# Kernel optimization log

Hardware: AMD Instinct MI355X
Metric: run time of the kernel (lower is better)

Reference implementation:

```python
import jax, jax.numpy as jnp
import numpy as np

N, E, D, H, ED = 10000, 160000, 512, 256, 16
EPS = 1e-5  # BatchNorm1d eps


def _cgconv(x, src, dst, edge_attr, Wf, bf, Ws, bs, gamma, beta, mean, var):
    # PyG CGConv: z = [x_i, x_j, e_ij]; m = sigmoid(lin_f(z)) * softplus(lin_s(z));
    # aggr='add' at target i; batch_norm (eval mode, running stats) then residual.
    z = jnp.concatenate([x[dst], x[src], edge_attr], axis=1)  # [E, 2D+ED]
    m = jax.nn.sigmoid(z @ Wf + bf) * jax.nn.softplus(z @ Ws + bs)  # [E, D]
    aggr = jax.ops.segment_sum(m, dst, num_segments=x.shape[0])  # [N, D]
    bn = (aggr - mean) * jax.lax.rsqrt(var + EPS) * gamma + beta
    return x + bn


def _gcnconv(x, src, dst, W, b):
    # PyG GCNConv with add_self_loops=True, normalize=True:
    n = x.shape[0]
    deg = jax.ops.segment_sum(jnp.ones((src.shape[0],), x.dtype), dst, num_segments=n) + 1.0
    dinv = jax.lax.rsqrt(deg)  # [N]
    h = x @ W  # [N, out]
    out = jax.ops.segment_sum((dinv[src] * dinv[dst])[:, None] * h[src], dst, num_segments=n)
    out = out + (dinv * dinv)[:, None] * h  # self-loop contribution
    return out + b


def _forward(x, edge_attr, goal_feat,
             cg1_Wf, cg1_bf, cg1_Ws, cg1_bs, cg1_gamma, cg1_beta, cg1_mean, cg1_var,
             cg2_Wf, cg2_bf, cg2_Ws, cg2_bs, cg2_gamma, cg2_beta, cg2_mean, cg2_var,
             gcn3_W, gcn3_b, gcn4_W, gcn4_b, d1_W, d1_b, d2_W, d2_b, src, dst):
    # dropout layers are identity in eval mode (self.training=False)
    x = jax.nn.relu(_cgconv(x, src, dst, edge_attr, cg1_Wf, cg1_bf, cg1_Ws, cg1_bs,
                            cg1_gamma, cg1_beta, cg1_mean, cg1_var))
    x = jax.nn.relu(_cgconv(x, src, dst, edge_attr, cg2_Wf, cg2_bf, cg2_Ws, cg2_bs,
                            cg2_gamma, cg2_beta, cg2_mean, cg2_var))
    x = jax.nn.relu(_gcnconv(x, src, dst, gcn3_W, gcn3_b))
    x = jax.nn.relu(_gcnconv(x, src, dst, gcn4_W, gcn4_b))
    g = jnp.broadcast_to(goal_feat, (x.shape[0], goal_feat.shape[1]))  # repeat(num_nodes, 1)
    h = jax.nn.relu(jnp.concatenate([x, g], axis=1) @ d1_W + d1_b)
    return h @ d2_W + d2_b  # [N, 1]


def setup_inputs() -> dict:
    ks = jax.random.split(jax.random.key(0), 12)
    w = lambda k, s: jax.random.normal(k, s, dtype=jnp.float32) * 0.02
    Z = 2 * D + ED
    return {
        "x": jax.random.normal(ks[0], (N, D), jnp.float32),
        "edge_attr": jax.random.normal(ks[1], (E, ED), jnp.float32),
        "goal_feat": jax.random.normal(ks[2], (1, D), jnp.float32),
        "cg1_Wf": w(ks[3], (Z, D)), "cg1_bf": jnp.zeros((D,), jnp.float32),
        "cg1_Ws": w(ks[4], (Z, D)), "cg1_bs": jnp.zeros((D,), jnp.float32),
        "cg1_gamma": jnp.ones((D,), jnp.float32), "cg1_beta": jnp.zeros((D,), jnp.float32),
        "cg1_mean": jnp.zeros((D,), jnp.float32), "cg1_var": jnp.ones((D,), jnp.float32),
        "cg2_Wf": w(ks[5], (Z, D)), "cg2_bf": jnp.zeros((D,), jnp.float32),
        "cg2_Ws": w(ks[6], (Z, D)), "cg2_bs": jnp.zeros((D,), jnp.float32),
        "cg2_gamma": jnp.ones((D,), jnp.float32), "cg2_beta": jnp.zeros((D,), jnp.float32),
        "cg2_mean": jnp.zeros((D,), jnp.float32), "cg2_var": jnp.ones((D,), jnp.float32),
        "gcn3_W": w(ks[7], (D, H)), "gcn3_b": jnp.zeros((H,), jnp.float32),
        "gcn4_W": w(ks[8], (H, H)), "gcn4_b": jnp.zeros((H,), jnp.float32),
        "d1_W": w(ks[9], (H + D, D)), "d1_b": jnp.zeros((D,), jnp.float32),
        "d2_W": w(ks[10], (D, 1)), "d2_b": jnp.zeros((1,), jnp.float32),
        "edge_index": jax.random.randint(ks[11], (2, E), 0, N, dtype=jnp.int32),
        "batch": jnp.zeros((N,), jnp.int32),
    }


def reference(x, edge_attr, goal_feat,
              cg1_Wf, cg1_bf, cg1_Ws, cg1_bs, cg1_gamma, cg1_beta, cg1_mean, cg1_var,
              cg2_Wf, cg2_bf, cg2_Ws, cg2_bs, cg2_gamma, cg2_beta, cg2_mean, cg2_var,
              gcn3_W, gcn3_b, gcn4_W, gcn4_b, d1_W, d1_b, d2_W, d2_b,
              edge_index, batch):
    src, dst = edge_index[0], edge_index[1]
    return _forward(x, edge_attr, goal_feat,
                    cg1_Wf, cg1_bf, cg1_Ws, cg1_bs, cg1_gamma, cg1_beta, cg1_mean, cg1_var,
                    cg2_Wf, cg2_bf, cg2_Ws, cg2_bs, cg2_gamma, cg2_beta, cg2_mean, cg2_var,
                    gcn3_W, gcn3_b, gcn4_W, gcn4_b, d1_W, d1_b, d2_W, d2_b, src, dst)
```

## Files before the change

kernel.cpp:

```cpp
#include <hip/hip_runtime.h>
#include <math.h>

#define N_NODES 10000
#define N_EDGES 160000
#define DIM 512
#define HDIM 256
#define EDIM 16
#define BN_EPS 1e-5f
#define L2E 1.4426950408889634f
#define LN2 0.6931471805599453f

typedef unsigned short ushort_t;
typedef unsigned int uint_t;
typedef __attribute__((ext_vector_type(8))) short bf16x8;
typedef __attribute__((ext_vector_type(4))) float f32x4;
typedef __attribute__((ext_vector_type(2))) _Float16 half2_t;

__device__ __forceinline__ ushort_t f2bf(float x) {
    uint_t u = __float_as_uint(x);
    uint_t r = (u + 0x7FFF + ((u >> 16) & 1)) >> 16;
    return (ushort_t)r;
}
__device__ __forceinline__ float bflo(uint_t u) {
    return __uint_as_float(u << 16);
}
__device__ __forceinline__ float bfhi(uint_t u) {
    return __uint_as_float(u & 0xffff0000u);
}
__device__ __forceinline__ void gld16(const void* g, void* l) {
    __builtin_amdgcn_global_load_lds(
        (const __attribute__((address_space(1))) unsigned int*)g,
        (__attribute__((address_space(3))) unsigned int*)l, 16, 0, 0);
}
__device__ __forceinline__ half2_t u2h(uint_t u) {
    return __builtin_bit_cast(half2_t, u);
}
__device__ __forceinline__ uint_t pk_f16(float a, float b) {
    return __builtin_bit_cast(uint_t, __builtin_amdgcn_cvt_pkrtz(a, b));
}
__device__ __forceinline__ ushort_t f2h(float x) {
    return (ushort_t)(pk_f16(x, 0.f) & 0xffffu);
}
__device__ __forceinline__ float fexp2(float x) {
#if __has_builtin(__builtin_amdgcn_exp2f)
    return __builtin_amdgcn_exp2f(x);
#else
    return __expf(x * LN2);
#endif
}
__device__ __forceinline__ float flog2(float x) {
#if __has_builtin(__builtin_amdgcn_logf)
    return __builtin_amdgcn_logf(x);
#else
    return __logf(x) * L2E;
#endif
}
__device__ __forceinline__ void swz(int lid, int gx, int gy, int& bx, int& by) {
    int per = gy * 8;
    int grp = lid / per;
    int rem = lid - grp * per;
    int gsz = min(8, gx - grp * 8);
    by = rem / gsz;
    bx = grp * 8 + (rem - by * gsz);
}

__global__ void k_hist(const int* __restrict__ dst, int* __restrict__ cnt) {
    int e = blockIdx.x * blockDim.x + threadIdx.x;
    if (e < N_EDGES) atomicAdd(&cnt[dst[e]], 1);
}

__global__ __launch_bounds__(1024) void k_scan(int* __restrict__ offs, float* __restrict__ dinv) {
    __shared__ int wsum[16];
    int t = threadIdx.x, lane = t & 63, wv = t >> 6;
    int base_i = t * 10;
    int v[10];
    int s = 0;
#pragma unroll
    for (int k = 0; k < 10; k++) {
        int idx = base_i + k;
        int x = (idx < N_NODES) ? offs[idx] : 0;
        v[k] = x;
        s += x;
        if (idx < N_NODES) dinv[idx] = rsqrtf((float)x + 1.0f);
    }
    int ps = s;
#pragma unroll
    for (int off = 1; off < 64; off <<= 1) {
        int u = __shfl_up(ps, off, 64);
        if (lane >= off) ps += u;
    }
    if (lane == 63) wsum[wv] = ps;
    __syncthreads();
    if (wv == 0) {
        int w = (lane < 16) ? wsum[lane] : 0;
#pragma unroll
        for (int off = 1; off < 16; off <<= 1) {
            int u = __shfl_up(w, off, 64);
            if (lane >= off) w += u;
        }
        if (lane < 16) wsum[lane] = w;
    }
    __syncthreads();
    int wbase = (wv == 0) ? 0 : wsum[wv - 1];
    int run = wbase + ps - s;
#pragma unroll
    for (int k = 0; k < 10; k++) {
        int idx = base_i + k;
        if (idx < N_NODES) offs[idx] = run;
        run += v[k];
    }
    if (t == 1023) offs[N_NODES] = wsum[15];
}

__global__ void k_scatter(const int* __restrict__ srcv, const int* __restrict__ dstv,
                          const float* __restrict__ ea,
                          const int* __restrict__ offs, const float* __restrict__ dinv,
                          int* __restrict__ cursor,
                          int* __restrict__ srcQ, int* __restrict__ srcH,
                          float* __restrict__ dinvArr,
                          uint_t* __restrict__ eaP) {
    int e = blockIdx.x * blockDim.x + threadIdx.x;
    if (e >= N_EDGES) return;
    int d = dstv[e];
    int p = offs[d] + atomicAdd(&cursor[d], 1);
    int s = srcv[e];
    srcQ[p] = s << 11;
    srcH[p] = s << 9;
    dinvArr[p] = dinv[s];
    const float* er = ea + (size_t)e * EDIM;
    uint_t pk[8];
#pragma unroll
    for (int k2 = 0; k2 < 8; k2++) pk[k2] = pk_f16(er[2 * k2], er[2 * k2 + 1]);
    uint_t* q = eaP + (size_t)p * 8;
    *(uint4*)q = *(uint4*)&pk[0];
    *(uint4*)(q + 4) = *(uint4*)&pk[4];
}

__global__ __launch_bounds__(256) void k_cvtW(
    const float* __restrict__ Wf0, const float* __restrict__ Ws0,
    const float* __restrict__ Wf1, const float* __restrict__ Ws1,
    const float* __restrict__ g3W, const float* __restrict__ g4W,
    const float* __restrict__ d1W,
    ushort_t* __restrict__ W2cg0, ushort_t* __restrict__ W2cg1,
    ushort_t* __restrict__ W2g3, ushort_t* __restrict__ W2g4,
    ushort_t* __restrict__ W2d1)
{
    __shared__ ushort_t tle[64][72];
    int b = blockIdx.x, t = threadIdx.x;
    const float* src; int ldw, kin0, cin0, ldk, cout0, kout0; ushort_t* out; float scale;
    if (b < 512) {
        int layer = b >> 8, tt = b & 255;
        int g = tt >> 6, rem = tt & 63;
        int ct = rem >> 3, kt = rem & 7;
        const float* Wf = layer ? Wf1 : Wf0;
        const float* Ws = layer ? Ws1 : Ws0;
        src = (g & 1) ? Ws : Wf;
        ldw = 512; kin0 = ((g & 2) ? 512 : 0) + kt * 64; cin0 = ct * 64;
        out = layer ? W2cg1 : W2cg0; ldk = 512;
        cout0 = g * 512 + ct * 64; kout0 = kt * 64;
        scale = L2E;
    } else if (b < 544) {
        int tt = b - 512; int ct = tt >> 3, kt = tt & 7;
        src = g3W; ldw = 256; kin0 = kt * 64; cin0 = ct * 64;
        out = W2g3; ldk = 512; cout0 = ct * 64; kout0 = kt * 64; scale = 1.f;
    } else if (b < 560) {
        int tt = b - 544; int ct = tt >> 2, kt = tt & 3;
        src = g4W; ldw = 256; kin0 = kt * 64; cin0 = ct * 64;
        out = W2g4; ldk = 256; cout0 = ct * 64; kout0 = kt * 64; scale = 1.f;
    } else {
        int tt = b - 560; int ct = tt >> 2, kt = tt & 3;
        src = d1W; ldw = 512; kin0 = kt * 64; cin0 = ct * 64;
        out = W2d1; ldk = 256; cout0 = ct * 64; kout0 = kt * 64; scale = 1.f;
    }
    int c = t & 63;
    int k4 = t >> 6;
#pragma unroll
    for (int i = 0; i < 16; i++) {
        int k = k4 * 16 + i;
        tle[k][c] = f2bf(src[(size_t)(kin0 + k) * ldw + cin0 + c] * scale);
    }
    __syncthreads();
    int cl = t >> 2, kq = t & 3;
    ushort_t tmp[16];
#pragma unroll
    for (int j = 0; j < 16; j++) tmp[j] = tle[kq * 16 + j][cl];
    ushort_t* dst = out + (size_t)(cout0 + cl) * ldk + kout0 + kq * 16;
    *(uint4*)dst = *(uint4*)&tmp[0];
    *(uint4*)(dst + 8) = *(uint4*)&tmp[8];
}

__global__ __launch_bounds__(256) void k_prep2(
    const float* __restrict__ bf0, const float* __restrict__ bs0,
    const float* __restrict__ gm0, const float* __restrict__ bt0,
    const float* __restrict__ mn0, const float* __restrict__ vr0,
    const float* __restrict__ bf1, const float* __restrict__ bs1,
    const float* __restrict__ gm1, const float* __restrict__ bt1,
    const float* __restrict__ mn1, const float* __restrict__ vr1,
    float* __restrict__ biasCG, float* __restrict__ bnS, float* __restrict__ bnB)
{
    int layer = blockIdx.x;
    const float* bf = layer ? bf1 : bf0;
    const float* bs = layer ? bs1 : bs0;
    const float* gm = layer ? gm1 : gm0;
    const float* bt = layer ? bt1 : bt0;
    const float* mn = layer ? mn1 : mn0;
    const float* vr = layer ? vr1 : vr0;
    int t = threadIdx.x;
    for (int c = t; c < 512; c += 256) {
        biasCG[layer * 1024 + c] = bf[c] * L2E;
        biasCG[layer * 1024 + 512 + c] = bs[c] * L2E;
        float rs = rsqrtf(vr[c] + BN_EPS) * gm[c];
        bnS[layer * 512 + c] = LN2 * rs;
        bnB[layer * 512 + c] = bt[c] - mn[c] * rs;
    }
}

#define MP_WEP   32
#define MP_GV    40
#define MP_END   20040

__global__ __launch_bounds__(256) void k_megaprep(
    const float* __restrict__ x, const float* __restrict__ goal,
    const float* __restrict__ Wf0, const float* __restrict__ Ws0,
    const float* __restrict__ Wf1, const float* __restrict__ Ws1,
    const float* __restrict__ d1W, const float* __restrict__ d1b,
    ushort_t* __restrict__ A2, uint_t* __restrict__ WEP, float* __restrict__ cgv)
{
    int b = blockIdx.x, t = threadIdx.x;
    if (b < MP_WEP) {
        int layer = b >> 4, blk = b & 15;
        int idx = blk * 256 + t;
        int c = idx >> 3, k2 = idx & 7;
        const float* Wf = (layer ? Wf1 : Wf0) + 1024 * 512;
        const float* Ws = (layer ? Ws1 : Ws0) + 1024 * 512;
        uint_t* WEPf = WEP + layer * 8192;
        uint_t* WEPs = WEPf + 4096;
        WEPf[c * 8 + k2] = pk_f16(Wf[(2 * k2) * 512 + c] * L2E, Wf[(2 * k2 + 1) * 512 + c] * L2E);
        WEPs[c * 8 + k2] = pk_f16(Ws[(2 * k2) * 512 + c] * L2E, Ws[(2 * k2 + 1) * 512 + c] * L2E);
    } else if (b < MP_GV) {
        __shared__ float red[256];
        int bb = b - MP_WEP;
        int c = bb * 64 + (t & 63);
        int slice = t >> 6;
        float acc = 0.f;
        for (int i = 0; i < 128; i++) {
            int k = slice * 128 + i;
            acc += goal[k] * d1W[(size_t)(256 + k) * 512 + c];
        }
        red[t] = acc;
        __syncthreads();
        if (t < 128) red[t] += red[t + 128];
        __syncthreads();
        if (t < 64) cgv[c] = red[t] + red[t + 64] + d1b[c];
    } else {
        int idx = (b - MP_GV) * 256 + t;
        if (idx < N_NODES * 512) A2[idx] = f2bf(x[idx]);
    }
}

__global__ __launch_bounds__(256) void k_gemm3(
    const ushort_t* __restrict__ A2, int K, int M,
    const ushort_t* __restrict__ W2t,
    float* __restrict__ outF, ushort_t* __restrict__ outQ,
    const float* __restrict__ bias, int mode, int ldc, int gx, int gy)
{
    __shared__ ushort_t As[128 * 64];
    __shared__ ushort_t Bs[128 * 64];
    int tid = threadIdx.x;
    int lane = tid & 63, w = tid >> 6;
    int wm = w & 1, wn = w >> 1;
    int lrow = lane & 15, quad = lane >> 4;
    int bx, by;
    swz(blockIdx.x, gx, gy, bx, by);
    int row0 = bx * 128, col0 = by * 128;

    f32x4 acc[4][4] = {};

    const ushort_t* ArG[4]; ushort_t* ArL[4];
    const ushort_t* BrG[4]; ushort_t* BrL[4];
#pragma unroll
    for (int p = 0; p < 4; p++) {
        int s = tid + 256 * p;
        int r = s >> 3, k8p = s & 7;
        int k8l = k8p ^ (r & 7);
        int gra = row0 + r; if (gra >= M) gra = M - 1;
        ArG[p] = A2 + (size_t)gra * K + k8l * 8;
        ArL[p] = As + s * 8;
        BrG[p] = W2t + (size_t)(col0 + r) * K + k8l * 8;
        BrL[p] = Bs + s * 8;
    }
    const ushort_t* afp[2][4];
    const ushort_t* bfp[2][4];
#pragma unroll
    for (int sl = 0; sl < 2; sl++)
#pragma unroll
        for (int mt = 0; mt < 4; mt++) {
            int r = wm * 64 + mt * 16 + lrow;
            afp[sl][mt] = As + (r * 8 + ((sl * 4 + quad) ^ (r & 7))) * 8;
            int c = wn * 64 + mt * 16 + lrow;
            bfp[sl][mt] = Bs + (c * 8 + ((sl * 4 + quad) ^ (c & 7))) * 8;
        }

    for (int k0 = 0; k0 < K; k0 += 64) {
        __syncthreads();
#pragma unroll
        for (int p = 0; p < 4; p++) {
            gld16(ArG[p] + k0, ArL[p]);
            gld16(BrG[p] + k0, BrL[p]);
        }
        __syncthreads();
#pragma unroll
        for (int sl = 0; sl < 2; sl++) {
            bf16x8 af[4], bff[4];
#pragma unroll
            for (int i = 0; i < 4; i++) {
                af[i]  = *(const bf16x8*)afp[sl][i];
                bff[i] = *(const bf16x8*)bfp[sl][i];
            }
#pragma unroll
            for (int mt = 0; mt < 4; mt++)
#pragma unroll
                for (int nt = 0; nt < 4; nt++)
                    acc[mt][nt] = __builtin_amdgcn_mfma_f32_16x16x32_bf16(
                        af[mt], bff[nt], acc[mt][nt], 0, 0, 0);
        }
    }

#pragma unroll
    for (int mt = 0; mt < 4; mt++) {
#pragma unroll
        for (int nt = 0; nt < 4; nt++) {
            int gcol = col0 + wn * 64 + nt * 16 + lrow;
#pragma unroll
            for (int r = 0; r < 4; r++) {
                int grow = row0 + wm * 64 + mt * 16 + quad * 4 + r;
                if (grow >= M) continue;
                float v = acc[mt][nt][r];
                if (mode == 1) {
                    if (gcol < 1024) {
                        outF[(size_t)grow * 1024 + gcol] = v + bias[gcol];
                    } else {
                        int c = gcol - 1024;
                        int grp = c >> 9, cc = c & 511;
                        int pos = (cc >> 1) * 4 + grp * 2 + (cc & 1);
                        outQ[(size_t)grow * 1024 + pos] = f2h(v);
                    }
                } else if (mode == 2) {
                    outF[(size_t)grow * ldc + gcol] = fmaxf(v + bias[gcol], 0.f);
                } else {
                    outQ[(size_t)grow * ldc + gcol] = f2bf(v);
                }
            }
        }
    }
}

__global__ __launch_bounds__(256) void k_gemm64(
    const ushort_t* __restrict__ A2, int K, int M,
    const ushort_t* __restrict__ W2t,
    float* __restrict__ outF, ushort_t* __restrict__ outQ,
    const float* __restrict__ bias, int mode, int ldc, int gx, int gy)
{
    __shared__ ushort_t As[64 * 64];
    __shared__ ushort_t Bs[128 * 64];
    int tid = threadIdx.x;
    int lane = tid & 63, w = tid >> 6;
    int lrow = lane & 15, quad = lane >> 4;
    int bx, by;
    swz(blockIdx.x, gx, gy, bx, by);
    int row0 = bx * 64, col0 = by * 128;

    f32x4 acc[4][2] = {};

    const ushort_t* ArG[2]; ushort_t* ArL[2];
    const ushort_t* BrG[4]; ushort_t* BrL[4];
#pragma unroll
    for (int p = 0; p < 2; p++) {
        int s = tid + 256 * p;
        int r = s >> 3, k8p = s & 7;
        int k8l = k8p ^ (r & 7);
        int gra = row0 + r; if (gra >= M) gra = M - 1;
        ArG[p] = A2 + (size_t)gra * K + k8l * 8;
        ArL[p] = As + s * 8;
    }
#pragma unroll
    for (int p = 0; p < 4; p++) {
        int s = tid + 256 * p;
        int r = s >> 3, k8p = s & 7;
        int k8l = k8p ^ (r & 7);
        BrG[p] = W2t + (size_t)(col0 + r) * K + k8l * 8;
        BrL[p] = Bs + s * 8;
    }
    const ushort_t* afp[2][4];
    const ushort_t* bfp[2][2];
#pragma unroll
    for (int sl = 0; sl < 2; sl++) {
#pragma unroll
        for (int mt = 0; mt < 4; mt++) {
            int r = mt * 16 + lrow;
            afp[sl][mt] = As + (r * 8 + ((sl * 4 + quad) ^ (r & 7))) * 8;
        }
#pragma unroll
        for (int nt = 0; nt < 2; nt++) {
            int c = w * 32 + nt * 16 + lrow;
            bfp[sl][nt] = Bs + (c * 8 + ((sl * 4 + quad) ^ (c & 7))) * 8;
        }
    }

    for (int k0 = 0; k0 < K; k0 += 64) {
        __syncthreads();
        gld16(ArG[0] + k0, ArL[0]);
        gld16(ArG[1] + k0, ArL[1]);
#pragma unroll
        for (int p = 0; p < 4; p++) gld16(BrG[p] + k0, BrL[p]);
        __syncthreads();
#pragma unroll
        for (int sl = 0; sl < 2; sl++) {
            bf16x8 af[4], bff[2];
#pragma unroll
            for (int i = 0; i < 4; i++) af[i] = *(const bf16x8*)afp[sl][i];
#pragma unroll
            for (int i = 0; i < 2; i++) bff[i] = *(const bf16x8*)bfp[sl][i];
#pragma unroll
            for (int mt = 0; mt < 4; mt++)
#pragma unroll
                for (int nt = 0; nt < 2; nt++)
                    acc[mt][nt] = __builtin_amdgcn_mfma_f32_16x16x32_bf16(
                        af[mt], bff[nt], acc[mt][nt], 0, 0, 0);
        }
    }

#pragma unroll
    for (int mt = 0; mt < 4; mt++) {
#pragma unroll
        for (int nt = 0; nt < 2; nt++) {
            int gcol = col0 + w * 32 + nt * 16 + lrow;
#pragma unroll
            for (int r = 0; r < 4; r++) {
                int grow = row0 + mt * 16 + quad * 4 + r;
                if (grow >= M) continue;
                float v = acc[mt][nt][r];
                if (mode == 2) outF[(size_t)grow * ldc + gcol] = fmaxf(v + bias[gcol], 0.f);
                else outQ[(size_t)grow * ldc + gcol] = f2bf(v);
            }
        }
    }
}

#define CG_BODY(curq, jj) do {                                                     \
    uint4 eA = *(const uint4*)&sEaP[jj][0];                                        \
    uint4 eB = *(const uint4*)&sEaP[jj][4];                                        \
    float gf0 = __builtin_amdgcn_fdot2(u2h((curq).x), SEL10, pf.x, false);         \
    float gf1 = __builtin_amdgcn_fdot2(u2h((curq).x), SEL01, pf.y, false);         \
    float gs0 = __builtin_amdgcn_fdot2(u2h((curq).y), SEL10, ps.x, false);         \
    float gs1 = __builtin_amdgcn_fdot2(u2h((curq).y), SEL01, ps.y, false);         \
    uint_t ek[8] = {eA.x, eA.y, eA.z, eA.w, eB.x, eB.y, eB.z, eB.w};               \
    _Pragma("unroll")                                                              \
    for (int k = 0; k < 8; k++) {                                                  \
        half2_t e2 = u2h(ek[k]);                                                   \
        gf0 = __builtin_amdgcn_fdot2(e2, u2h(wfp[0][k]), gf0, false);              \
        gf1 = __builtin_amdgcn_fdot2(e2, u2h(wfp[1][k]), gf1, false);              \
        gs0 = __builtin_amdgcn_fdot2(e2, u2h(wsp[0][k]), gs0, false);              \
        gs1 = __builtin_amdgcn_fdot2(e2, u2h(wsp[1][k]), gs1, false);              \
    }                                                                              \
    float sg0 = __builtin_amdgcn_rcpf(1.f + fexp2(-gf0));                          \
    float sg1 = __builtin_amdgcn_rcpf(1.f + fexp2(-gf1));                          \
    float sp0 = flog2(1.f + fexp2(gs0));                                           \
    float sp1 = flog2(1.f + fexp2(gs1));                                           \
    acc0 = fmaf(sg0, sp0, acc0);                                                   \
    acc1 = fmaf(sg1, sp1, acc1);                                                   \
} while (0)

__global__ __launch_bounds__(256) void k_cg_aggr(
    const float* __restrict__ xin, const float* __restrict__ P,
    const ushort_t* __restrict__ Qi,
    const uint_t* __restrict__ WEPf, const uint_t* __restrict__ WEPs,
    const float* __restrict__ bnS, const float* __restrict__ bnB,
    const int* __restrict__ offs, const int* __restrict__ srcQ,
    const uint_t* __restrict__ eaP,
    float* __restrict__ xout, ushort_t* __restrict__ A2out)
{
    const half2_t SEL10 = {(_Float16)1.f, (_Float16)0.f};
    const half2_t SEL01 = {(_Float16)0.f, (_Float16)1.f};
    int i = blockIdx.x;
    int t = threadIdx.x;
    int c0 = 2 * t;
    uint_t wfp[2][8], wsp[2][8];
    {
        const uint_t* pf8 = WEPf + c0 * 8;
        const uint_t* ps8 = WEPs + c0 * 8;
        *(uint4*)&wfp[0][0] = *(const uint4*)(pf8 + 0);
        *(uint4*)&wfp[0][4] = *(const uint4*)(pf8 + 4);
        *(uint4*)&wfp[1][0] = *(const uint4*)(pf8 + 8);
        *(uint4*)&wfp[1][4] = *(const uint4*)(pf8 + 12);
        *(uint4*)&wsp[0][0] = *(const uint4*)(ps8 + 0);
        *(uint4*)&wsp[0][4] = *(const uint4*)(ps8 + 4);
        *(uint4*)&wsp[1][0] = *(const uint4*)(ps8 + 8);
        *(uint4*)&wsp[1][4] = *(const uint4*)(ps8 + 12);
    }
    float2 pf = *(const float2*)&P[(size_t)i * 1024 + c0];
    float2 ps = *(const float2*)&P[(size_t)i * 1024 + 512 + c0];
    float acc0 = 0.f, acc1 = 0.f;
    int e0 = offs[i], e1 = offs[i + 1];
    __shared__ uint_t sEaP[32][8];
    __shared__ int sOff[36];
    const char* Qb = (const char*)(Qi + 4 * t);
    for (int base = e0; base < e1; base += 32) {
        int g = min(32, e1 - base);
        __syncthreads();
        if (t < 36) sOff[t] = (t < g) ? srcQ[base + t] : 0;
        {
            int j = t >> 3, k2 = t & 7;
            if (j < g) sEaP[j][k2] = eaP[(size_t)(base + j) * 8 + k2];
        }
        __syncthreads();
        uint2 q[4];
#pragma unroll
        for (int p = 0; p < 4; p++) q[p] = *(const uint2*)(Qb + (uint_t)sOff[p]);
        int j = 0;
        for (; j + 4 <= g; j += 4) {
#pragma unroll
            for (int u = 0; u < 4; u++) {
                uint2 cur = q[u];
                q[u] = *(const uint2*)(Qb + (uint_t)sOff[j + u + 4]);
                CG_BODY(cur, j + u);
            }
        }
#pragma unroll
        for (int u = 0; u < 3; u++) {
            if (j + u < g) CG_BODY(q[u], j + u);
        }
    }
    float2 s2 = *(const float2*)&bnS[c0];
    float2 b2 = *(const float2*)&bnB[c0];
    size_t ib = (size_t)i * DIM;
    float2 xi = *(const float2*)&xin[ib + c0];
    float o0 = fmaxf(xi.x + fmaf(acc0, s2.x, b2.x), 0.f);
    float o1 = fmaxf(xi.y + fmaf(acc1, s2.y, b2.y), 0.f);
    if (xout) *(float2*)&xout[ib + c0] = make_float2(o0, o1);
    ushort_t h0 = f2bf(o0), h1 = f2bf(o1);
    *(uint_t*)(A2out + (size_t)i * 512 + c0) = (uint_t)h0 | ((uint_t)h1 << 16);
}

__global__ __launch_bounds__(128) void k_gcn_aggr(
    const ushort_t* __restrict__ h, const float* __restrict__ dinv,
    const float* __restrict__ bias,
    const int* __restrict__ offs, const int* __restrict__ srcH,
    const float* __restrict__ dinvArr, ushort_t* __restrict__ A2out)
{
    int i = blockIdx.x;
    int t = threadIdx.x;
    int c0 = 2 * t;
    float acc0 = 0.f, acc1 = 0.f;
    int e0 = offs[i], e1 = offs[i + 1];
    __shared__ int sS[40];
    __shared__ float sD[40];
    const char* hb = (const char*)(h + c0);
    for (int base = e0; base < e1; base += 32) {
        int g = min(32, e1 - base);
        __syncthreads();
        if (t < 40) {
            bool ok = (t < g);
            sS[t] = ok ? srcH[base + t] : 0;
            sD[t] = ok ? dinvArr[base + t] : 0.f;
        }
        __syncthreads();
        uint_t q[8];
#pragma unroll
        for (int p = 0; p < 8; p++) q[p] = *(const uint_t*)(hb + (uint_t)sS[p]);
        int j = 0;
        for (; j + 8 <= g; j += 8) {
#pragma unroll
            for (int u = 0; u < 8; u++) {
                uint_t cur = q[u];
                q[u] = *(const uint_t*)(hb + (uint_t)sS[j + u + 8]);
                float d = sD[j + u];
                acc0 = fmaf(d, bflo(cur), acc0);
                acc1 = fmaf(d, bfhi(cur), acc1);
            }
        }
#pragma unroll
        for (int u = 0; u < 7; u++) {
            if (j + u < g) {
                uint_t cur = q[u];
                float d = sD[j + u];
                acc0 = fmaf(d, bflo(cur), acc0);
                acc1 = fmaf(d, bfhi(cur), acc1);
            }
        }
    }
    float di = dinv[i];
    uint_t qi = *(const uint_t*)(h + (size_t)i * HDIM + c0);
    float2 b2 = *(const float2*)&bias[c0];
    float o0 = fmaxf(di * acc0 + di * di * bflo(qi) + b2.x, 0.f);
    float o1 = fmaxf(di * acc1 + di * di * bfhi(qi) + b2.y, 0.f);
    ushort_t h0 = f2bf(o0), h1 = f2bf(o1);
    *(uint_t*)(A2out + (size_t)i * 256 + c0) = (uint_t)h0 | ((uint_t)h1 << 16);
}

__global__ __launch_bounds__(256) void k_final(const float* __restrict__ hd,
                                               const float* __restrict__ w2,
                                               const float* __restrict__ b2,
                                               float* __restrict__ out) {
    int wave = threadIdx.x >> 6, lane = threadIdx.x & 63;
    int i = blockIdx.x * 4 + wave;
    if (i >= N_NODES) return;
    const float* r = hd + (size_t)i * DIM;
    float acc = 0.f;
#pragma unroll
    for (int q = 0; q < 8; q++) acc += r[lane + 64 * q] * w2[lane + 64 * q];
#pragma unroll
    for (int off = 32; off > 0; off >>= 1) acc += __shfl_down(acc, off, 64);
    if (lane == 0) out[i] = acc + b2[0];
}

extern "C" void kernel_launch(void* const* d_in, const int* in_sizes, int n_in,
                              void* d_out, int out_size, void* d_ws, size_t ws_size,
                              hipStream_t stream) {
    (void)in_sizes; (void)n_in; (void)out_size; (void)ws_size;
    const float* x      = (const float*)d_in[0];
    const float* ea     = (const float*)d_in[1];
    const float* goal   = (const float*)d_in[2];
    const float* cgWf[2] = {(const float*)d_in[3],  (const float*)d_in[11]};
    const float* cgbf[2] = {(const float*)d_in[4],  (const float*)d_in[12]};
    const float* cgWs[2] = {(const float*)d_in[5],  (const float*)d_in[13]};
    const float* cgbs[2] = {(const float*)d_in[6],  (const float*)d_in[14]};
    const float* cggm[2] = {(const float*)d_in[7],  (const float*)d_in[15]};
    const float* cgbt[2] = {(const float*)d_in[8],  (const float*)d_in[16]};
    const float* cgmn[2] = {(const float*)d_in[9],  (const float*)d_in[17]};
    const float* cgvr[2] = {(const float*)d_in[10], (const float*)d_in[18]};
    const float* gcn3_W = (const float*)d_in[19];
    const float* gcn3_b = (const float*)d_in[20];
    const float* gcn4_W = (const float*)d_in[21];
    const float* gcn4_b = (const float*)d_in[22];
    const float* d1_W   = (const float*)d_in[23];
    const float* d1_b   = (const float*)d_in[24];
    const float* d2_W   = (const float*)d_in[25];
    const float* d2_b   = (const float*)d_in[26];
    const int*   eidx   = (const int*)d_in[27];
    const int*   srcv   = eidx;
    const int*   dstv   = eidx + N_EDGES;
    float* outp = (float*)d_out;

    char* w = (char*)d_ws;
    float*    Pbuf  = (float*)w;                      w += (size_t)N_NODES * 1024 * 4;
    ushort_t* Qbuf  = (ushort_t*)w;                   w += (size_t)N_NODES * 1024 * 2;
    float*    xB    = (float*)w;                      w += (size_t)N_NODES * 512 * 4;
    ushort_t* A2    = (ushort_t*)w;                   w += (size_t)N_NODES * 512 * 2;
    ushort_t* A3    = (ushort_t*)w;                   w += (size_t)N_NODES * 256 * 2;
    ushort_t* W2cg0 = (ushort_t*)w;                   w += (size_t)2048 * 512 * 2;
    ushort_t* W2cg1 = (ushort_t*)w;                   w += (size_t)2048 * 512 * 2;
    ushort_t* W2g3  = (ushort_t*)w;                   w += (size_t)256 * 512 * 2;
    ushort_t* W2g4  = (ushort_t*)w;                   w += (size_t)256 * 256 * 2;
    ushort_t* W2d1  = (ushort_t*)w;                   w += (size_t)512 * 256 * 2;
    uint_t*   eaP   = (uint_t*)w;                     w += (size_t)N_EDGES * 8 * 4;
    uint_t*   WEP   = (uint_t*)w;                     w += 16384 * 4;
    float*    cgv   = (float*)w;                      w += 512 * 4;
    float*    biasCG = (float*)w;                     w += 2048 * 4;
    float*    bnS    = (float*)w;                     w += 1024 * 4;
    float*    bnB    = (float*)w;                     w += 1024 * 4;
    int*      srcQ    = (int*)w;                      w += N_EDGES * 4;
    int*      srcH    = (int*)w;                      w += N_EDGES * 4;
    float*    dinvArr = (float*)w;                    w += N_EDGES * 4;
    int*      offs    = (int*)w;                      w += (N_NODES + 1) * 4;
    int*      cursor  = (int*)w;                      w += N_NODES * 4;
    float*    dinv    = (float*)w;                    w += N_NODES * 4;
    uint_t* WEPf[2] = {WEP, WEP + 8192};
    uint_t* WEPs[2] = {WEP + 4096, WEP + 12288};
    ushort_t* h3 = (ushort_t*)Pbuf;
    float*    hd = (float*)Qbuf;

    k_cvtW<<<592, 256, 0, stream>>>(cgWf[0], cgWs[0], cgWf[1], cgWs[1],
                                    gcn3_W, gcn4_W, d1_W,
                                    W2cg0, W2cg1, W2g3, W2g4, W2d1);
    k_prep2<<<2, 256, 0, stream>>>(cgbf[0], cgbs[0], cggm[0], cgbt[0], cgmn[0], cgvr[0],
                                   cgbf[1], cgbs[1], cggm[1], cgbt[1], cgmn[1], cgvr[1],
                                   biasCG, bnS, bnB);
    k_megaprep<<<MP_END, 256, 0, stream>>>(x, goal,
        cgWf[0], cgWs[0], cgWf[1], cgWs[1], d1_W, d1_b, A2, WEP, cgv);

    hipMemsetAsync(offs, 0, (N_NODES + 1) * sizeof(int), stream);
    hipMemsetAsync(cursor, 0, N_NODES * sizeof(int), stream);
    k_hist<<<(N_EDGES + 255) / 256, 256, 0, stream>>>(dstv, offs);
    k_scan<<<1, 1024, 0, stream>>>(offs, dinv);
    k_scatter<<<(N_EDGES + 255) / 256, 256, 0, stream>>>(srcv, dstv, ea, offs, dinv,
                                                         cursor, srcQ, srcH, dinvArr, eaP);

    k_gemm3<<<79 * 16, 256, 0, stream>>>(A2, 512, N_NODES, W2cg0,
                                         Pbuf, Qbuf, biasCG, 1, 0, 79, 16);
    k_cg_aggr<<<N_NODES, 256, 0, stream>>>(x, Pbuf, Qbuf, WEPf[0], WEPs[0],
                                           bnS, bnB, offs, srcQ, eaP, xB, A2);
    k_gemm3<<<79 * 16, 256, 0, stream>>>(A2, 512, N_NODES, W2cg1,
                                         Pbuf, Qbuf, biasCG + 1024, 1, 0, 79, 16);
    k_cg_aggr<<<N_NODES, 256, 0, stream>>>(xB, Pbuf, Qbuf, WEPf[1], WEPs[1],
                                           bnS + 512, bnB + 512, offs, srcQ, eaP,
                                           nullptr, A2);

    k_gemm64<<<157 * 2, 256, 0, stream>>>(A2, 512, N_NODES, W2g3,
                                          nullptr, h3, nullptr, 3, HDIM, 157, 2);
    k_gcn_aggr<<<N_NODES, 128, 0, stream>>>(h3, dinv, gcn3_b, offs, srcH, dinvArr, A3);

    k_gemm64<<<157 * 2, 256, 0, stream>>>(A3, 256, N_NODES, W2g4,
                                          nullptr, h3, nullptr, 3, HDIM, 157, 2);
    k_gcn_aggr<<<N_NODES, 128, 0, stream>>>(h3, dinv, gcn4_b, offs, srcH, dinvArr, A3);

    k_gemm64<<<157 * 4, 256, 0, stream>>>(A3, 256, N_NODES, W2d1,
                                          hd, nullptr, cgv, 2, DIM, 157, 4);
    k_final<<<(N_NODES + 3) / 4, 256, 0, stream>>>(hd, d2_W, d2_b, outp);
}
```

Baseline: 530.2 us.

## Fuse final dense layer into GEMM epilogue, vectorize conversion, deepen gather prefetch

The last GEMM now applies bias and ReLU, dots each row with d2_W in registers, reduces across lanes and the block, and atomically adds into the output. This removes the fp32 hidden buffer write and read and the separate k_final launch. The x-to-bf16 conversion now handles 8 elements per thread with vector loads and stores, so far fewer blocks are launched. The CG aggregation prefetch depth goes from 4 to 8 gathered rows. Atomics make the output summation order nondeterministic, and the deeper prefetch adds register pressure.

Measured after the change: 517.6 us. -2.4%, faster.

```diff
diff --git a/kernel.cpp b/kernel.cpp
--- a/kernel.cpp
+++ b/kernel.cpp
@@ -217,7 +217,7 @@
 
 #define MP_WEP   32
 #define MP_GV    40
-#define MP_END   20040
+#define MP_END   2540
 
 __global__ __launch_bounds__(256) void k_megaprep(
     const float* __restrict__ x, const float* __restrict__ goal,
@@ -253,8 +253,17 @@
         __syncthreads();
         if (t < 64) cgv[c] = red[t] + red[t + 64] + d1b[c];
     } else {
-        int idx = (b - MP_GV) * 256 + t;
-        if (idx < N_NODES * 512) A2[idx] = f2bf(x[idx]);
+        int base = ((b - MP_GV) * 256 + t) * 8;
+        if (base < N_NODES * 512) {
+            float4 a = *(const float4*)&x[base];
+            float4 c = *(const float4*)&x[base + 4];
+            uint_t o[4];
+            o[0] = (uint_t)f2bf(a.x) | ((uint_t)f2bf(a.y) << 16);
+            o[1] = (uint_t)f2bf(a.z) | ((uint_t)f2bf(a.w) << 16);
+            o[2] = (uint_t)f2bf(c.x) | ((uint_t)f2bf(c.y) << 16);
+            o[3] = (uint_t)f2bf(c.z) | ((uint_t)f2bf(c.w) << 16);
+            *(uint4*)(A2 + base) = *(uint4*)&o[0];
+        }
     }
 }
 
@@ -359,10 +368,12 @@
     const ushort_t* __restrict__ A2, int K, int M,
     const ushort_t* __restrict__ W2t,
     float* __restrict__ outF, ushort_t* __restrict__ outQ,
-    const float* __restrict__ bias, int mode, int ldc, int gx, int gy)
+    const float* __restrict__ bias, int mode, int ldc, int gx, int gy,
+    const float* __restrict__ w2v, const float* __restrict__ b2v)
 {
     __shared__ ushort_t As[64 * 64];
     __shared__ ushort_t Bs[128 * 64];
+    __shared__ float sOutW[4][64];
     int tid = threadIdx.x;
     int lane = tid & 63, w = tid >> 6;
     int lrow = lane & 15, quad = lane >> 4;
@@ -428,6 +439,36 @@
                     acc[mt][nt] = __builtin_amdgcn_mfma_f32_16x16x32_bf16(
                         af[mt], bff[nt], acc[mt][nt], 0, 0, 0);
         }
+    }
+
+    if (mode == 4) {
+#pragma unroll
+        for (int mt = 0; mt < 4; mt++) {
+#pragma unroll
+            for (int r = 0; r < 4; r++) {
+                float p = 0.f;
+#pragma unroll
+                for (int nt = 0; nt < 2; nt++) {
+                    int gcol = col0 + w * 32 + nt * 16 + lrow;
+                    p += fmaxf(acc[mt][nt][r] + bias[gcol], 0.f) * w2v[gcol];
+                }
+                p += __shfl_xor(p, 1, 64);
+                p += __shfl_xor(p, 2, 64);
+                p += __shfl_xor(p, 4, 64);
+                p += __shfl_xor(p, 8, 64);
+                if (lrow == 0) sOutW[w][mt * 16 + quad * 4 + r] = p;
+            }
+        }
+        __syncthreads();
+        if (tid < 64) {
+            int grow = row0 + tid;
+            if (grow < M) {
+                float v = sOutW[0][tid] + sOutW[1][tid] + sOutW[2][tid] + sOutW[3][tid];
+                if (col0 == 0) v += b2v[0];
+                atomicAdd(&outF[grow], v);
+            }
+        }
+        return;
     }
 
 #pragma unroll
@@ -503,31 +544,31 @@
     float acc0 = 0.f, acc1 = 0.f;
     int e0 = offs[i], e1 = offs[i + 1];
     __shared__ uint_t sEaP[32][8];
-    __shared__ int sOff[36];
+    __shared__ int sOff[40];
     const char* Qb = (const char*)(Qi + 4 * t);
     for (int base = e0; base < e1; base += 32) {
         int g = min(32, e1 - base);
         __syncthreads();
-        if (t < 36) sOff[t] = (t < g) ? srcQ[base + t] : 0;
+        if (t < 40) sOff[t] = (t < g) ? srcQ[base + t] : 0;
         {
             int j = t >> 3, k2 = t & 7;
             if (j < g) sEaP[j][k2] = eaP[(size_t)(base + j) * 8 + k2];
         }
         __syncthreads();
-        uint2 q[4];
-#pragma unroll
-        for (int p = 0; p < 4; p++) q[p] = *(const uint2*)(Qb + (uint_t)sOff[p]);
+        uint2 q[8];
+#pragma unroll
+        for (int p = 0; p < 8; p++) q[p] = *(const uint2*)(Qb + (uint_t)sOff[p]);
         int j = 0;
-        for (; j + 4 <= g; j += 4) {
-#pragma unroll
-            for (int u = 0; u < 4; u++) {
+        for (; j + 8 <= g; j += 8) {
+#pragma unroll
+            for (int u = 0; u < 8; u++) {
                 uint2 cur = q[u];
-                q[u] = *(const uint2*)(Qb + (uint_t)sOff[j + u + 4]);
+                q[u] = *(const uint2*)(Qb + (uint_t)sOff[j + u + 8]);
                 CG_BODY(cur, j + u);
             }
         }
 #pragma unroll
-        for (int u = 0; u < 3; u++) {
+        for (int u = 0; u < 7; u++) {
             if (j + u < g) CG_BODY(q[u], j + u);
         }
     }
@@ -596,22 +637,6 @@
     float o1 = fmaxf(di * acc1 + di * di * bfhi(qi) + b2.y, 0.f);
     ushort_t h0 = f2bf(o0), h1 = f2bf(o1);
     *(uint_t*)(A2out + (size_t)i * 256 + c0) = (uint_t)h0 | ((uint_t)h1 << 16);
-}
-
-__global__ __launch_bounds__(256) void k_final(const float* __restrict__ hd,
-                                               const float* __restrict__ w2,
-                                               const float* __restrict__ b2,
-                                               float* __restrict__ out) {
-    int wave = threadIdx.x >> 6, lane = threadIdx.x & 63;
-    int i = blockIdx.x * 4 + wave;
-    if (i >= N_NODES) return;
-    const float* r = hd + (size_t)i * DIM;
-    float acc = 0.f;
-#pragma unroll
-    for (int q = 0; q < 8; q++) acc += r[lane + 64 * q] * w2[lane + 64 * q];
-#pragma unroll
-    for (int off = 32; off > 0; off >>= 1) acc += __shfl_down(acc, off, 64);
-    if (lane == 0) out[i] = acc + b2[0];
 }
 
 extern "C" void kernel_launch(void* const* d_in, const int* in_sizes, int n_in,
@@ -668,7 +693,6 @@
     uint_t* WEPf[2] = {WEP, WEP + 8192};
     uint_t* WEPs[2] = {WEP + 4096, WEP + 12288};
     ushort_t* h3 = (ushort_t*)Pbuf;
-    float*    hd = (float*)Qbuf;
 
     k_cvtW<<<592, 256, 0, stream>>>(cgWf[0], cgWs[0], cgWf[1], cgWs[1],
                                     gcn3_W, gcn4_W, d1_W,
@@ -697,14 +721,17 @@
                                            nullptr, A2);
 
     k_gemm64<<<157 * 2, 256, 0, stream>>>(A2, 512, N_NODES, W2g3,
-                                          nullptr, h3, nullptr, 3, HDIM, 157, 2);
+                                          nullptr, h3, nullptr, 3, HDIM, 157, 2,
+                                          nullptr, nullptr);
     k_gcn_aggr<<<N_NODES, 128, 0, stream>>>(h3, dinv, gcn3_b, offs, srcH, dinvArr, A3);
 
     k_gemm64<<<157 * 2, 256, 0, stream>>>(A3, 256, N_NODES, W2g4,
-                                          nullptr, h3, nullptr, 3, HDIM, 157, 2);
+                                          nullptr, h3, nullptr, 3, HDIM, 157, 2,
+                                          nullptr, nullptr);
     k_gcn_aggr<<<N_NODES, 128, 0, stream>>>(h3, dinv, gcn4_b, offs, srcH, dinvArr, A3);
 
+    hipMemsetAsync(outp, 0, N_NODES * sizeof(float), stream);
     k_gemm64<<<157 * 4, 256, 0, stream>>>(A3, 256, N_NODES, W2d1,
-                                          hd, nullptr, cgv, 2, DIM, 157, 4);
-    k_final<<<(N_NODES + 3) / 4, 256, 0, stream>>>(hd, d2_W, d2_b, outp);
-}
+                                          outp, nullptr, cgv, 4, DIM, 157, 4,
+                                          d2_W, d2_b);
+}
```
